# Kernel tuning notes

Measured on AMD Instinct MI355X. Metric: run time of the kernel, lower is better.

Reference implementation:

```python
import jax, jax.numpy as jnp
import numpy as np

B, H, T, D = 2, 16, 2048, 64
BASE_WINDOW = 256
FULL = 999999


def _make_window_sizes(num_heads=H, base_window=BASE_WINDOW):
    ws = []
    for h in range(num_heads):
        if h < num_heads // 4:
            ws.append(base_window)
        elif h < num_heads // 2:
            ws.append(base_window * 2)
        elif h < 3 * num_heads // 4:
            ws.append(base_window * 4)
        else:
            ws.append(FULL)
    return jnp.asarray(ws, dtype=jnp.int32)


def setup_inputs() -> dict:
    key = jax.random.key(0)
    kq, kk, kv = jax.random.split(key, 3)
    Q = jax.random.normal(kq, (B, H, T, D), dtype=jnp.float32)
    K = jax.random.normal(kk, (B, H, T, D), dtype=jnp.float32)
    V = jax.random.normal(kv, (B, H, T, D), dtype=jnp.float32)
    return {"Q": Q, "K": K, "V": V, "window_sizes": _make_window_sizes()}


def reference(Q, K, V, window_sizes):
    b, h, t, d = Q.shape
    scale = 1.0 / np.sqrt(d).astype(np.float32)
    idx = jnp.arange(t, dtype=jnp.int32)
    diff = idx[:, None] - idx[None, :]  # [T, T], q_idx - kv_idx
    # causal & |q-k| <= w  ==  0 <= diff <= w  (per head)
    mask = (diff >= 0) & (diff[None, :, :] <= window_sizes[:, None, None])  # [H, T, T]
    scores = jnp.einsum('bhqd,bhkd->bhqk', Q, K) * scale  # [B, H, T, T]
    scores = jnp.where(mask[None], scores, -jnp.inf)
    attn = jax.nn.softmax(scores, axis=-1)
    return jnp.einsum('bhqk,bhkd->bhqd', attn, V)
```

## Files before the change

### kernel.cpp

```cpp
#include <hip/hip_runtime.h>
#include <hip/hip_bf16.h>


constexpr int Bc = 2, Hc = 16, Tc = 2048, Dc = 64;
constexpr int BQ = 64;
constexpr int BK = 32;
constexpr float QSCALE = 0.125f * 1.44269504088896340736f;
constexpr float CMAX = 16.0f;

constexpr size_t VB_OFF = 256;
constexpr int HEADE = Tc * Dc;

constexpr int KOFF = 0;
constexpr int VOFF = 8192;

typedef __attribute__((ext_vector_type(8))) short short8;
typedef __attribute__((ext_vector_type(4))) float float4v;
typedef __attribute__((ext_vector_type(2))) unsigned int uint2v;

#if defined(__has_builtin)
#if __has_builtin(__builtin_amdgcn_exp2f)
#define EXP2 __builtin_amdgcn_exp2f
#endif
#endif
#ifndef EXP2
#define EXP2 exp2f
#endif

__device__ inline unsigned f2bf_u(float f) {
    union { float f; unsigned u; } v; v.f = f;
    return (v.u + 0x7fffu + ((v.u >> 16) & 1u)) >> 16;
}

__device__ inline short8 pack8(const float* t) {
    short8 r;
#pragma unroll
    for (int j = 0; j < 8; j++) r[j] = (short)f2bf_u(t[j]);
    return r;
}

__device__ inline unsigned pk_bf16(float a, float b) {
    __hip_bfloat162 h = __float22bfloat162_rn(make_float2(a, b));
    union { __hip_bfloat162 h; unsigned u; } v; v.h = h;
    return v.u;
}

__device__ inline short8 mk8(unsigned a0, unsigned a1, unsigned a2, unsigned a3) {
    union { unsigned u[4]; short8 s; } v;
    v.u[0] = a0; v.u[1] = a1; v.u[2] = a2; v.u[3] = a3;
    return v.s;
}

__global__ __launch_bounds__(256)
void preconv_kernel(const float* __restrict__ V, unsigned short* __restrict__ Vtb) {
    __shared__ float tile[64][65];
    const int blk2 = blockIdx.x;
    const int tid = threadIdx.x;
    const int bh = blk2 >> 5;
    const int t0 = (blk2 & 31) * 64;
    const float* src = V + (size_t)bh * HEADE + (size_t)t0 * Dc;
#pragma unroll
    for (int i = 0; i < 4; i++) {
        const int r = (tid >> 4) + i * 16;
        const int d4 = (tid & 15) * 4;
        float4v v4 = *(const float4v*)(src + r * Dc + d4);
        tile[r][d4] = v4[0]; tile[r][d4 + 1] = v4[1];
        tile[r][d4 + 2] = v4[2]; tile[r][d4 + 3] = v4[3];
    }
    __syncthreads();
    unsigned short* dst = Vtb + (size_t)bh * HEADE + t0;
#pragma unroll
    for (int i = 0; i < 2; i++) {
        const int d = (tid >> 3) + 32 * i;
        const int c = tid & 7;
        float t[8];
#pragma unroll
        for (int j = 0; j < 8; j++) t[j] = tile[c * 8 + j][d];
        *(short8*)(dst + (size_t)d * Tc + c * 8) = pack8(t);
    }
}

__global__ __launch_bounds__(256, 4)
void dswa_kernel(const float* __restrict__ Q,
                 const float* __restrict__ K,
                 const unsigned short* __restrict__ Vtb,
                 const int* __restrict__ wsz,
                 float* __restrict__ O) {
    __shared__ __align__(16) unsigned short LDS[18432];

    const int tid  = threadIdx.x;
    const int wave = tid >> 6;
    const int g    = wave >> 1;
    const int wq   = wave & 1;
    const int lane = tid & 63;
    const int quad = lane >> 4;
    const int l16  = lane & 15;

    unsigned short* Kg = &LDS[KOFF + g * 4096];
    unsigned short* Vg = &LDS[VOFF + g * 5120];

    const int l128 = tid & 127;
    const int krow = l128 >> 2;
    const int kcol = (l128 & 3) * 16;
    const int vrow = l128 >> 1;
    const int vcol = (l128 & 1) * 16;

    const int blk  = blockIdx.x;
    const int ci   = blk & 255;
    const int slot = blk >> 8;
    const int b    = ci & 1;
    const int q5   = (ci >> 1) & 31;
    const int hh   = ci >> 6;
    const int h    = (3 - slot) * 4 + hh;
    const int qt   = (slot == 0) ? q5 : 31 - q5;
    const int q0   = qt * BQ;
    const int win  = wsz[h];

    const size_t headoff = (size_t)(b * Hc + h) * HEADE;
    const float* Qp = Q + headoff;
    const float* Kh = K + headoff;
    const unsigned short* Vbh = Vtb + headoff;
    float* Op = O + headoff;

    short8 qf[2][2];
#pragma unroll
    for (int s = 0; s < 2; s++) {
        const int qrow = q0 + wq * 32 + s * 16 + l16;
#pragma unroll
        for (int c = 0; c < 2; c++) {
            const float* src = Qp + (size_t)qrow * Dc + c * 32 + quad * 8;
            float4v a = *(const float4v*)src;
            float4v d4 = *(const float4v*)(src + 4);
            float t[8] = {a[0]*QSCALE, a[1]*QSCALE, a[2]*QSCALE, a[3]*QSCALE,
                          d4[0]*QSCALE, d4[1]*QSCALE, d4[2]*QSCALE, d4[3]*QSCALE};
            qf[s][c] = pack8(t);
        }
    }

    float4v acc[2][4];
#pragma unroll
    for (int s = 0; s < 2; s++)
#pragma unroll
        for (int nb = 0; nb < 4; nb++) acc[s][nb] = (float4v){0.f, 0.f, 0.f, 0.f};
    float lp0 = 0.0f, lp1 = 0.0f;

    const int kv_lo = (max(0, q0 - win)) & ~(BK - 1);
    const int n_tiles = (q0 + BQ - kv_lo) >> 5;
    const int IT = (n_tiles + 1) >> 1;

    const int kv0g = kv_lo + g * BK;
    const float* kgp = Kh + (size_t)(kv0g + krow) * Dc + kcol;
    const unsigned short* vgp = Vbh + (size_t)vrow * Tc + kv0g + vcol;

    float4v ka0, ka1, ka2, ka3;
    short8 vr0, vr1;
    if (g < n_tiles) {
        ka0 = *(const float4v*)(kgp);
        ka1 = *(const float4v*)(kgp + 4);
        ka2 = *(const float4v*)(kgp + 8);
        ka3 = *(const float4v*)(kgp + 12);
        vr0 = *(const short8*)(vgp);
        vr1 = *(const short8*)(vgp + 8);
    }
    kgp += 64 * Dc; vgp += 64;

    for (int t = 0; t < IT; ++t) {
        const int ti = g + 2 * t;
        const bool act = ti < n_tiles;
        const int kv0 = kv_lo + ti * BK;
        unsigned short* Kl = Kg + (t & 1) * 2048;
        unsigned short* Vt = Vg + (t & 1) * 2560;

        if (act) {
            const int ks = (krow & 7) << 3;
            short8 kr0 = mk8(pk_bf16(ka0[0], ka0[1]), pk_bf16(ka0[2], ka0[3]),
                             pk_bf16(ka1[0], ka1[1]), pk_bf16(ka1[2], ka1[3]));
            short8 kr1 = mk8(pk_bf16(ka2[0], ka2[1]), pk_bf16(ka2[2], ka2[3]),
                             pk_bf16(ka3[0], ka3[1]), pk_bf16(ka3[2], ka3[3]));
            *(short8*)&Kl[krow * 64 + (kcol ^ ks)] = kr0;
            *(short8*)&Kl[krow * 64 + ((kcol + 8) ^ ks)] = kr1;
            *(short8*)&Vt[vrow * 40 + vcol] = vr0;
            *(short8*)&Vt[vrow * 40 + vcol + 8] = vr1;
        }
        __syncthreads();

        if (ti + 2 < n_tiles) {
            ka0 = *(const float4v*)(kgp);
            ka1 = *(const float4v*)(kgp + 4);
            ka2 = *(const float4v*)(kgp + 8);
            ka3 = *(const float4v*)(kgp + 12);
            vr0 = *(const short8*)(vgp);
            vr1 = *(const short8*)(vgp + 8);
        }
        kgp += 64 * Dc; vgp += 64;

        if (act) {
            float4v sT0[2], sT1[2];
            __builtin_amdgcn_s_setprio(1);
#pragma unroll
            for (int mb = 0; mb < 2; mb++) {
                float4v c0 = {-CMAX, -CMAX, -CMAX, -CMAX};
                float4v c1 = {-CMAX, -CMAX, -CMAX, -CMAX};
#pragma unroll
                for (int ch = 0; ch < 2; ch++) {
                    const int row = mb * 16 + l16;
                    short8 kf = *(short8*)&Kl[row * 64 +
                                              ((ch * 32 + quad * 8) ^ ((row & 7) << 3))];
                    c0 = __builtin_amdgcn_mfma_f32_16x16x32_bf16(kf, qf[0][ch], c0, 0, 0, 0);
                    c1 = __builtin_amdgcn_mfma_f32_16x16x32_bf16(kf, qf[1][ch], c1, 0, 0, 0);
                }
                sT0[mb] = c0; sT1[mb] = c1;
            }
            __builtin_amdgcn_s_setprio(0);

            short8 pf0, pf1;
            {
                const int rs = q0 + wq * 32;
                const bool interior = (kv0 + 31 <= rs) && (rs + 15 - kv0 <= win);
                if (!interior) {
                    const int dbase = rs + l16 - kv0 - quad * 4;
#pragma unroll
                    for (int mb = 0; mb < 2; mb++)
#pragma unroll
                        for (int r = 0; r < 4; r++) {
                            const unsigned diff = (unsigned)(dbase - mb * 16 - r);
                            sT0[mb][r] = (diff <= (unsigned)win) ? sT0[mb][r] : -3.0e38f;
                        }
                }
                unsigned w[4];
#pragma unroll
                for (int mb = 0; mb < 2; mb++) {
                    float p0 = EXP2(sT0[mb][0]);
                    float p1 = EXP2(sT0[mb][1]);
                    float p2 = EXP2(sT0[mb][2]);
                    float p3 = EXP2(sT0[mb][3]);
                    lp0 += (p0 + p1) + (p2 + p3);
                    w[2 * mb]     = pk_bf16(p0, p1);
                    w[2 * mb + 1] = pk_bf16(p2, p3);
                }
                uint2v pa = __builtin_amdgcn_permlane32_swap(w[0], w[2], false, false);
                uint2v c02 = __builtin_amdgcn_permlane16_swap(pa[0], pa[1], false, false);
                uint2v pb = __builtin_amdgcn_permlane32_swap(w[1], w[3], false, false);
                uint2v c13 = __builtin_amdgcn_permlane16_swap(pb[0], pb[1], false, false);
                pf0 = mk8(c02[0], c13[0], c02[1], c13[1]);
            }
            {
                const int rs = q0 + wq * 32 + 16;
                const bool interior = (kv0 + 31 <= rs) && (rs + 15 - kv0 <= win);
                if (!interior) {
                    const int dbase = rs + l16 - kv0 - quad * 4;
#pragma unroll
                    for (int mb = 0; mb < 2; mb++)
#pragma unroll
                        for (int r = 0; r < 4; r++) {
                            const unsigned diff = (unsigned)(dbase - mb * 16 - r);
                            sT1[mb][r] = (diff <= (unsigned)win) ? sT1[mb][r] : -3.0e38f;
                        }
                }
                unsigned w[4];
#pragma unroll
                for (int mb = 0; mb < 2; mb++) {
                    float p0 = EXP2(sT1[mb][0]);
                    float p1 = EXP2(sT1[mb][1]);
                    float p2 = EXP2(sT1[mb][2]);
                    float p3 = EXP2(sT1[mb][3]);
                    lp1 += (p0 + p1) + (p2 + p3);
                    w[2 * mb]     = pk_bf16(p0, p1);
                    w[2 * mb + 1] = pk_bf16(p2, p3);
                }
                uint2v pa = __builtin_amdgcn_permlane32_swap(w[0], w[2], false, false);
                uint2v c02 = __builtin_amdgcn_permlane16_swap(pa[0], pa[1], false, false);
                uint2v pb = __builtin_amdgcn_permlane32_swap(w[1], w[3], false, false);
                uint2v c13 = __builtin_amdgcn_permlane16_swap(pb[0], pb[1], false, false);
                pf1 = mk8(c02[0], c13[0], c02[1], c13[1]);
            }

            __builtin_amdgcn_s_setprio(1);
#pragma unroll
            for (int nb = 0; nb < 4; nb++) {
                short8 vf = *(short8*)&Vt[(nb * 16 + l16) * 40 + quad * 8];
                acc[0][nb] = __builtin_amdgcn_mfma_f32_16x16x32_bf16(pf0, vf, acc[0][nb], 0, 0, 0);
                acc[1][nb] = __builtin_amdgcn_mfma_f32_16x16x32_bf16(pf1, vf, acc[1][nb], 0, 0, 0);
            }
            __builtin_amdgcn_s_setprio(0);
        }
    }

    lp0 += __shfl_xor(lp0, 16); lp0 += __shfl_xor(lp0, 32);
    lp1 += __shfl_xor(lp1, 16); lp1 += __shfl_xor(lp1, 32);

    __syncthreads();
    float* fl = (float*)LDS;
    if (g == 1) {
#pragma unroll
        for (int s = 0; s < 2; s++) {
            if (quad == 0) fl[(wq * 32 + s * 16 + l16) * 66 + 64] = (s ? lp1 : lp0);
#pragma unroll
            for (int r = 0; r < 4; r++) {
                const int row = wq * 32 + s * 16 + quad * 4 + r;
#pragma unroll
                for (int nb = 0; nb < 4; nb++)
                    fl[row * 66 + nb * 16 + l16] = acc[s][nb][r];
            }
        }
    }
    __syncthreads();
    if (g == 0) {
#pragma unroll
        for (int s = 0; s < 2; s++) {
            const float lps = s ? lp1 : lp0;
#pragma unroll
            for (int r = 0; r < 4; r++) {
                const int row = wq * 32 + s * 16 + quad * 4 + r;
                const float l0 = __shfl(lps, quad * 4 + r);
                const float lt = l0 + fl[row * 66 + 64];
                const float inv = 1.0f / lt;
                float* dst = Op + (size_t)(q0 + row) * Dc;
#pragma unroll
                for (int nb = 0; nb < 4; nb++)
                    dst[nb * 16 + l16] = (acc[s][nb][r] + fl[row * 66 + nb * 16 + l16]) * inv;
            }
        }
    }
}

extern "C" void kernel_launch(void* const* d_in, const int* in_sizes, int n_in,
                              void* d_out, int out_size, void* d_ws, size_t ws_size,
                              hipStream_t stream) {
    (void)in_sizes; (void)n_in; (void)ws_size; (void)out_size;
    const float* Q = (const float*)d_in[0];
    const float* K = (const float*)d_in[1];
    const float* V = (const float*)d_in[2];
    const int* wsz = (const int*)d_in[3];
    float* Out = (float*)d_out;

    unsigned short* Vtb = (unsigned short*)((char*)d_ws + VB_OFF);

    preconv_kernel<<<dim3(1024), dim3(256), 0, stream>>>(V, Vtb);
    dswa_kernel<<<dim3(1024), dim3(256), 0, stream>>>(Q, K, Vtb, wsz, Out);
}
```

Measured before the change: 119.3 us.

## Split long full-attention query tiles across two blocks and merge via atomic ticket

Splits the key range of the longest full-window query tiles (qt 16-31) across two workgroups, each writing partial unnormalized sums and row sums to a workspace scratch buffer. The block that arrives second, determined by an atomic ticket counter, merges both halves and writes the normalized output. It also reorders block dispatch into a longest-first schedule mixing head classes to balance load. This adds scratch traffic, an extra sync and fence, and flag resets in the preconvert kernel. Merging by plain summation relies on the fixed softmax offset (CMAX) used in both halves.

Result: slower. 194.6 us (+63.2%).

```diff
diff --git a/kernel.cpp b/kernel.cpp
--- a/kernel.cpp
+++ b/kernel.cpp
@@ -9,6 +9,9 @@
 constexpr float CMAX = 16.0f;
 
 constexpr size_t VB_OFF = 256;
+constexpr size_t FLAGS_OFF = VB_OFF + (size_t)Bc * Hc * Tc * Dc * 2;
+constexpr size_t MRG_OFF = FLAGS_OFF + 512;
+constexpr int MRG_STRIDE = 4160;
 constexpr int HEADE = Tc * Dc;
 
 constexpr int KOFF = 0;
@@ -52,10 +55,12 @@
 }
 
 __global__ __launch_bounds__(256)
-void preconv_kernel(const float* __restrict__ V, unsigned short* __restrict__ Vtb) {
+void preconv_kernel(const float* __restrict__ V, unsigned short* __restrict__ Vtb,
+                    int* __restrict__ flags) {
     __shared__ float tile[64][65];
     const int blk2 = blockIdx.x;
     const int tid = threadIdx.x;
+    if (blk2 == 0 && tid < 128) flags[tid] = 0;
     const int bh = blk2 >> 5;
     const int t0 = (blk2 & 31) * 64;
     const float* src = V + (size_t)bh * HEADE + (size_t)t0 * Dc;
@@ -85,8 +90,11 @@
                  const float* __restrict__ K,
                  const unsigned short* __restrict__ Vtb,
                  const int* __restrict__ wsz,
+                 int* __restrict__ flags,
+                 float* __restrict__ mrg,
                  float* __restrict__ O) {
     __shared__ __align__(16) unsigned short LDS[18432];
+    __shared__ int ticket_s;
 
     const int tid  = threadIdx.x;
     const int wave = tid >> 6;
@@ -105,16 +113,62 @@
     const int vrow = l128 >> 1;
     const int vcol = (l128 & 1) * 16;
 
-    const int blk  = blockIdx.x;
-    const int ci   = blk & 255;
-    const int slot = blk >> 8;
-    const int b    = ci & 1;
-    const int q5   = (ci >> 1) & 31;
-    const int hh   = ci >> 6;
-    const int h    = (3 - slot) * 4 + hh;
-    const int qt   = (slot == 0) ? q5 : 31 - q5;
-    const int q0   = qt * BQ;
-    const int win  = wsz[h];
+    const int blk = blockIdx.x;
+    int cls, qt, sub, part = 0;
+    {
+        const int i = blk;
+        if (i < 128) { cls = 1; qt = 31 - (i >> 3); sub = i & 7; }
+        else if (i < 464) {
+            const int j = i - 128, k = 16 - j / 48, r = j % 48;
+            if (r < 8)      { cls = 1; qt = k - 1; sub = r & 7; }
+            else if (r < 16){ cls = 0; qt = k - 1; sub = r & 7; }
+            else { const int s = r - 16, s2 = s & 15;
+                   cls = 0; qt = 2 * k - 2 + (s >> 4); sub = s2 >> 1; part = 1 + (s2 & 1); }
+        }
+        else if (i < 704) {
+            const int r = i - 464;
+            if (r < 8)      { cls = 1; qt = 8; sub = r & 7; }
+            else if (r < 16){ cls = 0; qt = 8; sub = r & 7; }
+            else if (r < 48){ const int s = r - 16, s2 = s & 15;
+                              cls = 0; qt = 16 + (s >> 4); sub = s2 >> 1; part = 1 + (s2 & 1); }
+            else            { cls = 2; qt = 8 + ((r - 48) >> 3); sub = r & 7; }
+        }
+        else if (i < 776) {
+            const int j = i - 704, k = 8 - j / 24, r = j % 24;
+            cls = (r < 8) ? 1 : (r < 16) ? 0 : 2;
+            qt = k - 1; sub = r & 7;
+        }
+        else if (i < 1024) {
+            const int r = i - 776;
+            if (r < 8)      { cls = 1; qt = 4; sub = r & 7; }
+            else if (r < 16){ cls = 0; qt = 4; sub = r & 7; }
+            else if (r < 24){ cls = 2; qt = 4; sub = r & 7; }
+            else            { cls = 3; qt = 4 + ((r - 24) >> 3); sub = r & 7; }
+        }
+        else {
+            const int j = i - 1024, k = 4 - j / 32, r = j % 32;
+            cls = (r < 8) ? 1 : (r < 16) ? 0 : (r < 24) ? 2 : 3;
+            qt = k - 1; sub = r & 7;
+        }
+    }
+    const int b  = sub & 1;
+    const int hh = sub >> 1;
+    const int h  = (3 - cls) * 4 + hh;
+    const int q0 = qt * BQ;
+    const int win = wsz[h];
+
+    int key_base, C;
+    if (part == 0) {
+        const int kv_lo = (max(0, q0 - win)) & ~(BK - 1);
+        key_base = kv_lo;
+        C = (q0 + BQ - kv_lo) >> 5;
+    } else {
+        const int N = 2 * qt + 2;
+        const int half = N >> 1;
+        key_base = (part == 2) ? half * BK : 0;
+        C = (part == 2) ? N - half : half;
+    }
+    const int IT = (C + 1) >> 1;
 
     const size_t headoff = (size_t)(b * Hc + h) * HEADE;
     const float* Qp = Q + headoff;
@@ -144,17 +198,13 @@
         for (int nb = 0; nb < 4; nb++) acc[s][nb] = (float4v){0.f, 0.f, 0.f, 0.f};
     float lp0 = 0.0f, lp1 = 0.0f;
 
-    const int kv_lo = (max(0, q0 - win)) & ~(BK - 1);
-    const int n_tiles = (q0 + BQ - kv_lo) >> 5;
-    const int IT = (n_tiles + 1) >> 1;
-
-    const int kv0g = kv_lo + g * BK;
+    const int kv0g = key_base + g * BK;
     const float* kgp = Kh + (size_t)(kv0g + krow) * Dc + kcol;
     const unsigned short* vgp = Vbh + (size_t)vrow * Tc + kv0g + vcol;
 
     float4v ka0, ka1, ka2, ka3;
     short8 vr0, vr1;
-    if (g < n_tiles) {
+    if (g < C) {
         ka0 = *(const float4v*)(kgp);
         ka1 = *(const float4v*)(kgp + 4);
         ka2 = *(const float4v*)(kgp + 8);
@@ -166,8 +216,8 @@
 
     for (int t = 0; t < IT; ++t) {
         const int ti = g + 2 * t;
-        const bool act = ti < n_tiles;
-        const int kv0 = kv_lo + ti * BK;
+        const bool act = ti < C;
+        const int kv0 = key_base + ti * BK;
         unsigned short* Kl = Kg + (t & 1) * 2048;
         unsigned short* Vt = Vg + (t & 1) * 2560;
 
@@ -184,7 +234,7 @@
         }
         __syncthreads();
 
-        if (ti + 2 < n_tiles) {
+        if (ti + 2 < C) {
             ka0 = *(const float4v*)(kgp);
             ka1 = *(const float4v*)(kgp + 4);
             ka2 = *(const float4v*)(kgp + 8);
@@ -305,20 +355,71 @@
         }
     }
     __syncthreads();
-    if (g == 0) {
-#pragma unroll
-        for (int s = 0; s < 2; s++) {
-            const float lps = s ? lp1 : lp0;
-#pragma unroll
-            for (int r = 0; r < 4; r++) {
-                const int row = wq * 32 + s * 16 + quad * 4 + r;
-                const float l0 = __shfl(lps, quad * 4 + r);
-                const float lt = l0 + fl[row * 66 + 64];
-                const float inv = 1.0f / lt;
-                float* dst = Op + (size_t)(q0 + row) * Dc;
-#pragma unroll
-                for (int nb = 0; nb < 4; nb++)
-                    dst[nb * 16 + l16] = (acc[s][nb][r] + fl[row * 66 + nb * 16 + l16]) * inv;
+
+    if (part == 0) {
+        if (g == 0) {
+#pragma unroll
+            for (int s = 0; s < 2; s++) {
+                const float lps = s ? lp1 : lp0;
+#pragma unroll
+                for (int r = 0; r < 4; r++) {
+                    const int row = wq * 32 + s * 16 + quad * 4 + r;
+                    const float l0 = __shfl(lps, quad * 4 + r);
+                    const float lt = l0 + fl[row * 66 + 64];
+                    const float inv = 1.0f / lt;
+                    float* dst = Op + (size_t)(q0 + row) * Dc;
+#pragma unroll
+                    for (int nb = 0; nb < 4; nb++)
+                        dst[nb * 16 + l16] = (acc[s][nb][r] + fl[row * 66 + nb * 16 + l16]) * inv;
+                }
+            }
+        }
+    } else {
+        const int m = ((qt - 16) << 3) | sub;
+        float* scr = mrg + ((size_t)m * 2 + (part - 1)) * MRG_STRIDE;
+        if (g == 0) {
+#pragma unroll
+            for (int s = 0; s < 2; s++) {
+                const float lps = s ? lp1 : lp0;
+#pragma unroll
+                for (int r = 0; r < 4; r++) {
+                    const int row = wq * 32 + s * 16 + quad * 4 + r;
+                    const float l0 = __shfl(lps, quad * 4 + r);
+                    const float lt = l0 + fl[row * 66 + 64];
+#pragma unroll
+                    for (int nb = 0; nb < 4; nb++)
+                        scr[row * 65 + nb * 16 + l16] =
+                            acc[s][nb][r] + fl[row * 66 + nb * 16 + l16];
+                    if (l16 == 0) scr[row * 65 + 64] = lt;
+                }
+            }
+        }
+        __threadfence();
+        __syncthreads();
+        if (tid == 0)
+            ticket_s = __hip_atomic_fetch_add(&flags[m], 1, __ATOMIC_ACQ_REL,
+                                              __HIP_MEMORY_SCOPE_AGENT);
+        __syncthreads();
+        if (ticket_s == 1) {
+            __threadfence();
+            const float* sa = mrg + (size_t)m * 2 * MRG_STRIDE;
+            const float* sb = sa + MRG_STRIDE;
+            if (g == 0) {
+#pragma unroll
+                for (int s = 0; s < 2; s++) {
+#pragma unroll
+                    for (int r = 0; r < 4; r++) {
+                        const int row = wq * 32 + s * 16 + quad * 4 + r;
+                        const float lt = sa[row * 65 + 64] + sb[row * 65 + 64];
+                        const float inv = 1.0f / lt;
+                        float* dst = Op + (size_t)(q0 + row) * Dc;
+#pragma unroll
+                        for (int nb = 0; nb < 4; nb++)
+                            dst[nb * 16 + l16] =
+                                (sa[row * 65 + nb * 16 + l16] +
+                                 sb[row * 65 + nb * 16 + l16]) * inv;
+                    }
+                }
             }
         }
     }
@@ -335,7 +436,9 @@
     float* Out = (float*)d_out;
 
     unsigned short* Vtb = (unsigned short*)((char*)d_ws + VB_OFF);
-
-    preconv_kernel<<<dim3(1024), dim3(256), 0, stream>>>(V, Vtb);
-    dswa_kernel<<<dim3(1024), dim3(256), 0, stream>>>(Q, K, Vtb, wsz, Out);
-}
+    int* flags = (int*)((char*)d_ws + FLAGS_OFF);
+    float* mrg = (float*)((char*)d_ws + MRG_OFF);
+
+    preconv_kernel<<<dim3(1024), dim3(256), 0, stream>>>(V, Vtb, flags);
+    dswa_kernel<<<dim3(1152), dim3(256), 0, stream>>>(Q, K, Vtb, wsz, flags, mrg, Out);
+}
```

## Split long full-window query tiles across two blocks with a merge kernel

Applied to the files above, without the earlier changes.

The longest-running blocks (full-window heads, query tiles 16-31) now split their key range in half. Each half goes to a separate block, 1024 original slots plus 128 extra. Each half writes its unnormalized accumulator and row sum to workspace, and a new merge kernel sums the halves and normalizes. This is meant to shorten the tail caused by the heaviest blocks, at the cost of an extra launch, scratch traffic and more blocks. Combining the halves without rescaling relies on the fixed CMAX offset rather than a running max.

After: 128.8 us. 8.0% more time.

```diff
diff --git a/kernel.cpp b/kernel.cpp
--- a/kernel.cpp
+++ b/kernel.cpp
@@ -9,6 +9,8 @@
 constexpr float CMAX = 16.0f;
 
 constexpr size_t VB_OFF = 256;
+constexpr size_t MRG_OFF = VB_OFF + (size_t)Bc * Hc * Tc * Dc * 2;
+constexpr int MRG_STRIDE = 4352;
 constexpr int HEADE = Tc * Dc;
 
 constexpr int KOFF = 0;
@@ -85,6 +87,7 @@
                  const float* __restrict__ K,
                  const unsigned short* __restrict__ Vtb,
                  const int* __restrict__ wsz,
+                 float* __restrict__ mrg,
                  float* __restrict__ O) {
     __shared__ __align__(16) unsigned short LDS[18432];
 
@@ -105,16 +108,39 @@
     const int vrow = l128 >> 1;
     const int vcol = (l128 & 1) * 16;
 
-    const int blk  = blockIdx.x;
-    const int ci   = blk & 255;
-    const int slot = blk >> 8;
-    const int b    = ci & 1;
-    const int q5   = (ci >> 1) & 31;
-    const int hh   = ci >> 6;
-    const int h    = (3 - slot) * 4 + hh;
-    const int qt   = (slot == 0) ? q5 : 31 - q5;
-    const int q0   = qt * BQ;
-    const int win  = wsz[h];
+    const int blk = blockIdx.x;
+    int b, hh, h, qt, part = 0;
+    if (blk < 1024) {
+        const int ci   = blk & 255;
+        const int slot = blk >> 8;
+        b  = ci & 1;
+        hh = ci >> 6;
+        const int q5 = (ci >> 1) & 31;
+        h  = (3 - slot) * 4 + hh;
+        qt = (slot == 0) ? q5 : 31 - q5;
+        if (slot == 0 && qt >= 16) part = 1;
+    } else {
+        const int i = blk - 1024;
+        qt = 16 + (i >> 3);
+        hh = (i >> 1) & 3;
+        b  = i & 1;
+        h  = 12 + hh;
+        part = 2;
+    }
+    const int q0  = qt * BQ;
+    const int win = wsz[h];
+
+    int key_base, C;
+    if (part == 0) {
+        const int kv_lo = (max(0, q0 - win)) & ~(BK - 1);
+        key_base = kv_lo;
+        C = (q0 + BQ - kv_lo) >> 5;
+    } else {
+        const int half = qt + 1;
+        key_base = (part == 2) ? half * BK : 0;
+        C = half;
+    }
+    const int IT = (C + 1) >> 1;
 
     const size_t headoff = (size_t)(b * Hc + h) * HEADE;
     const float* Qp = Q + headoff;
@@ -144,17 +170,13 @@
         for (int nb = 0; nb < 4; nb++) acc[s][nb] = (float4v){0.f, 0.f, 0.f, 0.f};
     float lp0 = 0.0f, lp1 = 0.0f;
 
-    const int kv_lo = (max(0, q0 - win)) & ~(BK - 1);
-    const int n_tiles = (q0 + BQ - kv_lo) >> 5;
-    const int IT = (n_tiles + 1) >> 1;
-
-    const int kv0g = kv_lo + g * BK;
+    const int kv0g = key_base + g * BK;
     const float* kgp = Kh + (size_t)(kv0g + krow) * Dc + kcol;
     const unsigned short* vgp = Vbh + (size_t)vrow * Tc + kv0g + vcol;
 
     float4v ka0, ka1, ka2, ka3;
     short8 vr0, vr1;
-    if (g < n_tiles) {
+    if (g < C) {
         ka0 = *(const float4v*)(kgp);
         ka1 = *(const float4v*)(kgp + 4);
         ka2 = *(const float4v*)(kgp + 8);
@@ -166,8 +188,8 @@
 
     for (int t = 0; t < IT; ++t) {
         const int ti = g + 2 * t;
-        const bool act = ti < n_tiles;
-        const int kv0 = kv_lo + ti * BK;
+        const bool act = ti < C;
+        const int kv0 = key_base + ti * BK;
         unsigned short* Kl = Kg + (t & 1) * 2048;
         unsigned short* Vt = Vg + (t & 1) * 2560;
 
@@ -184,7 +206,7 @@
         }
         __syncthreads();
 
-        if (ti + 2 < n_tiles) {
+        if (ti + 2 < C) {
             ka0 = *(const float4v*)(kgp);
             ka1 = *(const float4v*)(kgp + 4);
             ka2 = *(const float4v*)(kgp + 8);
@@ -305,22 +327,70 @@
         }
     }
     __syncthreads();
-    if (g == 0) {
-#pragma unroll
-        for (int s = 0; s < 2; s++) {
-            const float lps = s ? lp1 : lp0;
-#pragma unroll
-            for (int r = 0; r < 4; r++) {
-                const int row = wq * 32 + s * 16 + quad * 4 + r;
-                const float l0 = __shfl(lps, quad * 4 + r);
-                const float lt = l0 + fl[row * 66 + 64];
-                const float inv = 1.0f / lt;
-                float* dst = Op + (size_t)(q0 + row) * Dc;
-#pragma unroll
-                for (int nb = 0; nb < 4; nb++)
-                    dst[nb * 16 + l16] = (acc[s][nb][r] + fl[row * 66 + nb * 16 + l16]) * inv;
-            }
-        }
+
+    if (part == 0) {
+        if (g == 0) {
+#pragma unroll
+            for (int s = 0; s < 2; s++) {
+                const float lps = s ? lp1 : lp0;
+#pragma unroll
+                for (int r = 0; r < 4; r++) {
+                    const int row = wq * 32 + s * 16 + quad * 4 + r;
+                    const float l0 = __shfl(lps, quad * 4 + r);
+                    const float lt = l0 + fl[row * 66 + 64];
+                    const float inv = 1.0f / lt;
+                    float* dst = Op + (size_t)(q0 + row) * Dc;
+#pragma unroll
+                    for (int nb = 0; nb < 4; nb++)
+                        dst[nb * 16 + l16] = (acc[s][nb][r] + fl[row * 66 + nb * 16 + l16]) * inv;
+                }
+            }
+        }
+    } else {
+        const int m = ((qt - 16) << 3) | (hh << 1) | b;
+        float* scr = mrg + ((size_t)m * 2 + (part - 1)) * MRG_STRIDE;
+        if (g == 0) {
+#pragma unroll
+            for (int s = 0; s < 2; s++) {
+                const float lps = s ? lp1 : lp0;
+#pragma unroll
+                for (int r = 0; r < 4; r++) {
+                    const int row = wq * 32 + s * 16 + quad * 4 + r;
+                    const float l0 = __shfl(lps, quad * 4 + r);
+                    const float lt = l0 + fl[row * 66 + 64];
+#pragma unroll
+                    for (int nb = 0; nb < 4; nb++)
+                        scr[row * 68 + nb * 16 + l16] =
+                            acc[s][nb][r] + fl[row * 66 + nb * 16 + l16];
+                    if (l16 == 0) scr[row * 68 + 64] = lt;
+                }
+            }
+        }
+    }
+}
+
+__global__ __launch_bounds__(256)
+void merge_kernel(const float* __restrict__ mrg, float* __restrict__ O) {
+    const int m = blockIdx.x;
+    const int qt = 16 + (m >> 3);
+    const int hh = (m >> 1) & 3;
+    const int b  = m & 1;
+    const int h  = 12 + hh;
+    const float* sa = mrg + (size_t)m * 2 * MRG_STRIDE;
+    const float* sb = sa + MRG_STRIDE;
+    const int row = threadIdx.x >> 2;
+    const int c0  = (threadIdx.x & 3) * 16;
+    const float lt = sa[row * 68 + 64] + sb[row * 68 + 64];
+    const float inv = 1.0f / lt;
+    float* dst = O + ((size_t)(b * Hc + h) * Tc + qt * BQ + row) * Dc + c0;
+#pragma unroll
+    for (int j = 0; j < 16; j += 4) {
+        float4v a = *(const float4v*)(sa + row * 68 + c0 + j);
+        float4v bb = *(const float4v*)(sb + row * 68 + c0 + j);
+        float4v o;
+        o[0] = (a[0] + bb[0]) * inv; o[1] = (a[1] + bb[1]) * inv;
+        o[2] = (a[2] + bb[2]) * inv; o[3] = (a[3] + bb[3]) * inv;
+        *(float4v*)(dst + j) = o;
     }
 }
 
@@ -335,7 +405,9 @@
     float* Out = (float*)d_out;
 
     unsigned short* Vtb = (unsigned short*)((char*)d_ws + VB_OFF);
+    float* mrg = (float*)((char*)d_ws + MRG_OFF);
 
     preconv_kernel<<<dim3(1024), dim3(256), 0, stream>>>(V, Vtb);
-    dswa_kernel<<<dim3(1024), dim3(256), 0, stream>>>(Q, K, Vtb, wsz, Out);
-}
+    dswa_kernel<<<dim3(1152), dim3(256), 0, stream>>>(Q, K, Vtb, wsz, mrg, Out);
+    merge_kernel<<<dim3(128), dim3(256), 0, stream>>>(mrg, Out);
+}
```
